# Optimization experiments

Hardware: AMD Instinct MI355X
Metric: run time of the kernel (lower is better)

Reference implementation:

```python
import jax, jax.numpy as jnp
import numpy as np

B, S, ENC = 16, 1500, 1280      # batch, audio frames, encoder dim
K = 2                            # pool stride -> in_dim = ENC*K
IN_DIM = ENC * K                 # 2560
LLM = 2048                       # output dim
HID = 512                        # expert hidden dim
E, TOPK = 8, 2                   # num experts, top-k
EPS = 1e-6


def _ln(x, g, b):
    m = jnp.mean(x, -1, keepdims=True)
    v = jnp.mean((x - m) ** 2, -1, keepdims=True)
    return (x - m) * jax.lax.rsqrt(v + EPS) * g + b


def _swiglu(x, w12, w3):
    # w12: [2H, D], w3: [O, H]; dropout is identity at inference
    h = x @ w12.T
    gate, val = jnp.split(h, 2, axis=-1)
    return (jax.nn.silu(gate) * val) @ w3.T


def setup_inputs() -> dict:
    key = jax.random.key(0)
    ks = jax.random.split(key, 12)
    sc = 0.02
    return {
        "x": jax.random.normal(ks[0], (B, S, ENC), jnp.float32),
        "ln_pre_g": 1.0 + sc * jax.random.normal(ks[1], (IN_DIM,), jnp.float32),
        "ln_pre_b": sc * jax.random.normal(ks[2], (IN_DIM,), jnp.float32),
        "router_w": sc * jax.random.normal(ks[3], (E, IN_DIM), jnp.float32),
        "router_b": sc * jax.random.normal(ks[4], (E,), jnp.float32),
        "shared_w12": sc * jax.random.normal(ks[5], (2 * HID, IN_DIM), jnp.float32),
        "shared_w3": sc * jax.random.normal(ks[6], (LLM, HID), jnp.float32),
        "experts_w12": sc * jax.random.normal(ks[7], (E, 2 * HID, IN_DIM), jnp.float32),
        "experts_w3": sc * jax.random.normal(ks[8], (E, LLM, HID), jnp.float32),
        "ln_post_g": 1.0 + sc * jax.random.normal(ks[9], (LLM,), jnp.float32),
        "ln_post_b": sc * jax.random.normal(ks[10], (LLM,), jnp.float32),
    }


def reference(x, ln_pre_g, ln_pre_b, router_w, router_b,
              shared_w12, shared_w3, experts_w12, experts_w3,
              ln_post_g, ln_post_b):
    b, s, d = x.shape
    pad = (-s) % K
    if pad:
        x = jnp.pad(x, ((0, 0), (0, pad), (0, 0)))
    xk = x.reshape(b, -1, d * K)          # [B, S/K, IN_DIM]
    new_s = xk.shape[1]
    nx = _ln(xk.reshape(-1, d * K), ln_pre_g, ln_pre_b)   # [T, IN_DIM]

    shared = _swiglu(nx, shared_w12, shared_w3)            # [T, LLM]

    logits = nx @ router_w.T + router_b                    # [T, E]
    probs = jax.nn.softmax(logits, -1)
    w, idx = jax.lax.top_k(probs, TOPK)                    # [T, K]
    w = w / (jnp.sum(w, -1, keepdims=True) + 1e-20)
    # combine[t, e] = sum_k w[t,k] * (idx[t,k]==e)  (equiv to masked loop + scatter-add)
    combine = jnp.sum(jax.nn.one_hot(idx, E, dtype=nx.dtype) * w[..., None], axis=1)  # [T, E]

    hid = jnp.einsum('td,efd->tef', nx, experts_w12)       # [T, E, 2H]
    gate, val = jnp.split(hid, 2, axis=-1)
    act = jax.nn.silu(gate) * val                          # [T, E, H]
    eo = jnp.einsum('teh,eoh->teo', act, experts_w3)       # [T, E, LLM]
    routed = jnp.einsum('teo,te->to', eo, combine)         # [T, LLM]

    out = _ln(shared + routed, ln_post_g, ln_post_b)
    return out.reshape(b, new_s, LLM)
```

## Files before the change

kernel.cpp:

```cpp
#include <hip/hip_runtime.h>

#define T_TOK 12000
#define NSLOT 24000
#define DIN 2560
#define DH 512
#define DOUT 2048
#define NEXP 8
#define MSH 12000
#define SHBASE 24000

typedef unsigned short u16;
typedef unsigned int u32;
typedef __attribute__((ext_vector_type(4))) float f32x4;
typedef __attribute__((ext_vector_type(8))) short short8;
typedef __attribute__((ext_vector_type(4))) u16 u16x4;
typedef __attribute__((ext_vector_type(8))) u16 u16x8;

__device__ __forceinline__ u16 f2bf(float f) {
  u32 u = __builtin_bit_cast(u32, f);
  return (u16)((u + 0x7fffu + ((u >> 16) & 1u)) >> 16);
}
__device__ __forceinline__ float bf2f(u16 h) {
  return __builtin_bit_cast(float, (u32)h << 16);
}

__device__ __forceinline__ void gload_lds16(const void* g, void* l) {
  __builtin_amdgcn_global_load_lds((const __attribute__((address_space(1))) u32*)g,
                                   (__attribute__((address_space(3))) u32*)l, 16, 0, 0);
}

__global__ __launch_bounds__(256) void cvt_bf16_kernel(const float* __restrict__ in,
                                                       u16* __restrict__ out, int n4) {
  const int i = blockIdx.x * 256 + threadIdx.x;
  if (i >= n4) return;
  f32x4 v = ((const f32x4*)in)[i];
  u16x4 o = { f2bf(v.x), f2bf(v.y), f2bf(v.z), f2bf(v.w) };
  ((u16x4*)out)[i] = o;
}

__global__ __launch_bounds__(256) void ln_router_kernel(
    const float* __restrict__ x, const float* __restrict__ gamma, const float* __restrict__ beta,
    const float* __restrict__ rw, const float* __restrict__ rb,
    u16* __restrict__ nx, int* __restrict__ tok_e, float* __restrict__ tok_w,
    int* __restrict__ count) {
  const int t = blockIdx.x * 4 + (threadIdx.x >> 6);
  const int lane = threadIdx.x & 63;
  const f32x4* xrow = (const f32x4*)(x + (size_t)t * DIN);

  f32x4 xv[10];
  float s = 0.f, s2 = 0.f;
#pragma unroll
  for (int c = 0; c < 10; ++c) {
    xv[c] = xrow[c * 64 + lane];
#pragma unroll
    for (int i = 0; i < 4; ++i) { s += xv[c][i]; s2 += xv[c][i] * xv[c][i]; }
  }
#pragma unroll
  for (int off = 32; off > 0; off >>= 1) {
    s += __shfl_xor(s, off);
    s2 += __shfl_xor(s2, off);
  }
  const float mean = s * (1.0f / DIN);
  const float var = s2 * (1.0f / DIN) - mean * mean;
  const float rstd = rsqrtf(var + 1e-6f);

  u16* nxrow = nx + (size_t)t * DIN;
#pragma unroll
  for (int c = 0; c < 10; ++c) {
    f32x4 g = ((const f32x4*)gamma)[c * 64 + lane];
    f32x4 b = ((const f32x4*)beta)[c * 64 + lane];
    xv[c] = (xv[c] - mean) * rstd * g + b;
    u16x4 p = { f2bf(xv[c].x), f2bf(xv[c].y), f2bf(xv[c].z), f2bf(xv[c].w) };
    ((u16x4*)nxrow)[c * 64 + lane] = p;
  }

  float lp[NEXP];
#pragma unroll
  for (int e = 0; e < NEXP; ++e) {
    const f32x4* rwe = (const f32x4*)(rw + (size_t)e * DIN);
    float acc = 0.f;
#pragma unroll
    for (int c = 0; c < 10; ++c) {
      f32x4 r = rwe[c * 64 + lane];
      acc += xv[c].x * r.x + xv[c].y * r.y + xv[c].z * r.z + xv[c].w * r.w;
    }
    lp[e] = acc;
  }
#pragma unroll
  for (int e = 0; e < NEXP; ++e)
#pragma unroll
    for (int off = 32; off > 0; off >>= 1) lp[e] += __shfl_xor(lp[e], off);

  if (lane == 0) {
    float lg[NEXP];
#pragma unroll
    for (int e = 0; e < NEXP; ++e) lg[e] = lp[e] + rb[e];
    float mx = lg[0];
#pragma unroll
    for (int e = 1; e < NEXP; ++e) mx = fmaxf(mx, lg[e]);
    float p[NEXP], ps = 0.f;
#pragma unroll
    for (int e = 0; e < NEXP; ++e) { p[e] = expf(lg[e] - mx); ps += p[e]; }
    int i0 = 0;
#pragma unroll
    for (int e = 1; e < NEXP; ++e) if (p[e] > p[i0]) i0 = e;
    int i1 = (i0 == 0) ? 1 : 0;
#pragma unroll
    for (int e = 0; e < NEXP; ++e) if (e != i0 && p[e] > p[i1]) i1 = e;
    float w0 = p[i0] / ps, w1 = p[i1] / ps;
    const float inv = 1.0f / (w0 + w1 + 1e-20f);
    w0 *= inv; w1 *= inv;
    tok_e[2 * t] = i0; tok_e[2 * t + 1] = i1;
    tok_w[2 * t] = w0; tok_w[2 * t + 1] = w1;
    atomicAdd(&count[i0 * 32], 1);
    atomicAdd(&count[i1 * 32], 1);
  }
}

__global__ void prefix_kernel(const int* __restrict__ count, int* __restrict__ prefix) {
  if (threadIdx.x == 0) {
    int acc = 0;
    for (int e = 0; e < NEXP; ++e) { prefix[e] = acc; acc += count[e * 32]; }
  }
}

__global__ __launch_bounds__(256) void assign_kernel(
    const int* __restrict__ tok_e, const float* __restrict__ tok_w, const int* __restrict__ prefix,
    int* __restrict__ cursor, int* __restrict__ slot_token, float* __restrict__ slot_w,
    int* __restrict__ token_slot) {
  const int t = blockIdx.x * 256 + threadIdx.x;
  if (t >= T_TOK) return;
#pragma unroll
  for (int k = 0; k < 2; ++k) {
    const int e = tok_e[2 * t + k];
    const int pos = atomicAdd(&cursor[e * 32], 1);
    const int sl = prefix[e] + pos;
    slot_token[sl] = t;
    slot_w[sl] = tok_w[2 * t + k];
    token_slot[2 * t + k] = sl;
  }
}

__global__ __launch_bounds__(256, 2) void gemm_ffn1(
    const u16* __restrict__ A0, const u16* __restrict__ Bsh, const u16* __restrict__ Bex,
    u16* __restrict__ ACT,
    const int* __restrict__ cnt32, const int* __restrict__ prefix,
    const int* __restrict__ slot_token) {
  constexpr int K = 2560;
  constexpr int NX = 8;
  __shared__ u16 ldsA[128 * 64];
  __shared__ u16 ldsG[64 * 64];
  __shared__ u16 ldsV[64 * 64];

  int A_act = 0;
#pragma unroll
  for (int ee = 0; ee < 9; ++ee) {
    const int c = (ee == 8) ? MSH : cnt32[ee * 32];
    A_act += ((c + 127) >> 7) * NX;
  }
  const int bid = blockIdx.x;
  if (bid >= A_act) return;

  const int xcd = bid & 7, rank = bid >> 3;
  const int q = A_act >> 3, r = A_act & 7;
  const int tile = (xcd < r ? xcd * (q + 1) : r * (q + 1) + (xcd - r) * q) + rank;

  int e = 8, local = 0, m_valid = MSH, row_off = 0;
  {
    int bacc = 0, found = 0;
#pragma unroll
    for (int ee = 0; ee < 9; ++ee) {
      const int c = (ee == 8) ? MSH : cnt32[ee * 32];
      const int w = ((c + 127) >> 7) * NX;
      if (!found && tile < bacc + w) {
        found = 1; e = ee; local = tile - bacc; m_valid = c;
        row_off = (ee == 8) ? 0 : prefix[ee];
      }
      bacc += w;
    }
  }
  const int ty = local / NX;
  const int tx = local % NX;
  const int crow_base = (e == 8) ? SHBASE : row_off;
  const u16* Bb = (e == 8) ? Bsh : Bex + (size_t)e * 1024 * K;

  const int tid = threadIdx.x;
  const int lane = tid & 63;
  const int wid = tid >> 6;
  const int sk8 = ((lane & 7) ^ (lane >> 3)) * 8;

  const u16* aptr[4];
#pragma unroll
  for (int i = 0; i < 4; ++i) {
    const int rr = wid * 32 + i * 8 + (lane >> 3);
    int gr = ty * 128 + rr;
    gr = gr < m_valid ? gr : (m_valid - 1);
    const int ar = (e == 8) ? gr : slot_token[row_off + gr];
    aptr[i] = A0 + (size_t)ar * K;
  }
  const u16* gptr[2];
  const u16* vptr[2];
#pragma unroll
  for (int j = 0; j < 2; ++j) {
    const int rr = wid * 16 + j * 8 + (lane >> 3);
    gptr[j] = Bb + (size_t)(tx * 64 + rr) * K;
    vptr[j] = Bb + (size_t)(512 + tx * 64 + rr) * K;
  }

  const f32x4 zero = {0.f, 0.f, 0.f, 0.f};
  f32x4 accg[4][2], accv[4][2];
#pragma unroll
  for (int m = 0; m < 4; ++m)
#pragma unroll
    for (int n = 0; n < 2; ++n) { accg[m][n] = zero; accv[m][n] = zero; }

  const int wr = (wid >> 1) * 64;
  const int wc = (wid & 1) * 32;
  const int fr = lane & 15;
  const int fk = (lane >> 4) * 8;

  for (int k0 = 0; k0 < K; k0 += 64) {
#pragma unroll
    for (int i = 0; i < 4; ++i)
      gload_lds16(aptr[i] + k0 + sk8, &ldsA[(wid * 4 + i) * 512]);
#pragma unroll
    for (int j = 0; j < 2; ++j) {
      gload_lds16(gptr[j] + k0 + sk8, &ldsG[(wid * 2 + j) * 512]);
      gload_lds16(vptr[j] + k0 + sk8, &ldsV[(wid * 2 + j) * 512]);
    }
    __syncthreads();
#pragma unroll
    for (int kk = 0; kk < 2; ++kk) {
      short8 af[4], bg[2], bv[2];
      const int kbs = (kk * 32 + fk) ^ ((lane & 7) << 3);
#pragma unroll
      for (int m = 0; m < 4; ++m)
        af[m] = *(const short8*)&ldsA[(wr + m * 16 + fr) * 64 + kbs];
#pragma unroll
      for (int n = 0; n < 2; ++n) {
        bg[n] = *(const short8*)&ldsG[(wc + n * 16 + fr) * 64 + kbs];
        bv[n] = *(const short8*)&ldsV[(wc + n * 16 + fr) * 64 + kbs];
      }
#pragma unroll
      for (int m = 0; m < 4; ++m)
#pragma unroll
        for (int n = 0; n < 2; ++n) {
          accg[m][n] = __builtin_amdgcn_mfma_f32_16x16x32_bf16(af[m], bg[n], accg[m][n], 0, 0, 0);
          accv[m][n] = __builtin_amdgcn_mfma_f32_16x16x32_bf16(af[m], bv[n], accv[m][n], 0, 0, 0);
        }
    }
    __syncthreads();
  }

  const int ccol = tx * 64 + wc + (lane & 15);
#pragma unroll
  for (int m = 0; m < 4; ++m) {
#pragma unroll
    for (int i = 0; i < 4; ++i) {
      const int row = wr + m * 16 + (lane >> 4) * 4 + i;
      const int gr = ty * 128 + row;
      if (gr < m_valid) {
        u16* crow = ACT + (size_t)(crow_base + gr) * DH;
#pragma unroll
        for (int n = 0; n < 2; ++n) {
          const float g = accg[m][n][i];
          const float v = accv[m][n][i];
          const float sig = 1.0f / (1.0f + __expf(-g));
          crow[ccol + n * 16] = f2bf(g * sig * v);
        }
      }
    }
  }
}

__global__ __launch_bounds__(256, 2) void gemm_ffn2(
    const u16* __restrict__ A0, const u16* __restrict__ Bsh, const u16* __restrict__ Bex,
    u16* __restrict__ C,
    const int* __restrict__ cnt32, const int* __restrict__ prefix,
    const float* __restrict__ slot_w) {
  constexpr int N = 2048;
  constexpr int K = 512;
  constexpr int NX = 16;
  __shared__ u16 ldsA[128 * 64];
  __shared__ u16 ldsB[128 * 64];

  int A_act = 0;
#pragma unroll
  for (int ee = 0; ee < 9; ++ee) {
    const int c = (ee == 8) ? MSH : cnt32[ee * 32];
    A_act += ((c + 127) >> 7) * NX;
  }
  const int bid = blockIdx.x;
  if (bid >= A_act) return;

  const int xcd = bid & 7, rank = bid >> 3;
  const int q = A_act >> 3, r = A_act & 7;
  const int tile = (xcd < r ? xcd * (q + 1) : r * (q + 1) + (xcd - r) * q) + rank;

  int e = 8, local = 0, m_valid = MSH, row_off = 0;
  {
    int bacc = 0, found = 0;
#pragma unroll
    for (int ee = 0; ee < 9; ++ee) {
      const int c = (ee == 8) ? MSH : cnt32[ee * 32];
      const int w = ((c + 127) >> 7) * NX;
      if (!found && tile < bacc + w) {
        found = 1; e = ee; local = tile - bacc; m_valid = c;
        row_off = (ee == 8) ? 0 : prefix[ee];
      }
      bacc += w;
    }
  }
  const int ty = local / NX;
  const int tx = local % NX;
  const int crow_base = (e == 8) ? SHBASE : row_off;
  const u16* Bb = (e == 8) ? Bsh : Bex + (size_t)e * N * K;

  const int tid = threadIdx.x;
  const int lane = tid & 63;
  const int wid = tid >> 6;
  const int sk8 = ((lane & 7) ^ (lane >> 3)) * 8;

  const u16* aptr[4];
  const u16* bptr[4];
#pragma unroll
  for (int i = 0; i < 4; ++i) {
    const int rr = wid * 32 + i * 8 + (lane >> 3);
    int gr = ty * 128 + rr;
    gr = gr < m_valid ? gr : (m_valid - 1);
    aptr[i] = A0 + (size_t)(crow_base + gr) * K;
    bptr[i] = Bb + (size_t)(tx * 128 + rr) * K;
  }

  const f32x4 zero = {0.f, 0.f, 0.f, 0.f};
  f32x4 acc[4][4];
#pragma unroll
  for (int m = 0; m < 4; ++m)
#pragma unroll
    for (int n = 0; n < 4; ++n) acc[m][n] = zero;

  const int wr = (wid >> 1) * 64;
  const int wc = (wid & 1) * 64;
  const int fr = lane & 15;
  const int fk = (lane >> 4) * 8;

  for (int k0 = 0; k0 < K; k0 += 64) {
#pragma unroll
    for (int i = 0; i < 4; ++i) {
      gload_lds16(aptr[i] + k0 + sk8, &ldsA[(wid * 4 + i) * 512]);
      gload_lds16(bptr[i] + k0 + sk8, &ldsB[(wid * 4 + i) * 512]);
    }
    __syncthreads();
#pragma unroll
    for (int kk = 0; kk < 2; ++kk) {
      short8 af[4], bfm[4];
      const int kbs = (kk * 32 + fk) ^ ((lane & 7) << 3);
#pragma unroll
      for (int m = 0; m < 4; ++m)
        af[m] = *(const short8*)&ldsA[(wr + m * 16 + fr) * 64 + kbs];
#pragma unroll
      for (int n = 0; n < 4; ++n)
        bfm[n] = *(const short8*)&ldsB[(wc + n * 16 + fr) * 64 + kbs];
#pragma unroll
      for (int m = 0; m < 4; ++m)
#pragma unroll
        for (int n = 0; n < 4; ++n)
          acc[m][n] = __builtin_amdgcn_mfma_f32_16x16x32_bf16(af[m], bfm[n], acc[m][n], 0, 0, 0);
    }
    __syncthreads();
  }

  const int ccol = wc + (lane & 15);
#pragma unroll
  for (int m = 0; m < 4; ++m) {
#pragma unroll
    for (int i = 0; i < 4; ++i) {
      const int row = wr + m * 16 + (lane >> 4) * 4 + i;
      const int gr = ty * 128 + row;
      if (gr < m_valid) {
        const float wscale = (e == 8) ? 1.0f : slot_w[row_off + gr];
        u16* crow = C + (size_t)(crow_base + gr) * N + tx * 128;
#pragma unroll
        for (int n = 0; n < 4; ++n) crow[ccol + n * 16] = f2bf(acc[m][n][i] * wscale);
      }
    }
  }
}

__global__ __launch_bounds__(256) void final_ln_kernel(
    const u16* __restrict__ O16, const int* __restrict__ token_slot,
    const float* __restrict__ gamma, const float* __restrict__ beta, float* __restrict__ out) {
  const int t = blockIdx.x;
  const int tid = threadIdx.x;
  const int lane = tid & 63;
  const int wv = tid >> 6;
  const int s0 = token_slot[2 * t], s1 = token_slot[2 * t + 1];
  const int c = tid * 8;
  u16x8 a8 = *(const u16x8*)&O16[(size_t)(SHBASE + t) * DOUT + c];
  u16x8 b8 = *(const u16x8*)&O16[(size_t)s0 * DOUT + c];
  u16x8 c8 = *(const u16x8*)&O16[(size_t)s1 * DOUT + c];
  float v[8];
  float s = 0.f, s2 = 0.f;
#pragma unroll
  for (int i = 0; i < 8; ++i) {
    v[i] = bf2f(a8[i]) + bf2f(b8[i]) + bf2f(c8[i]);
    s += v[i];
    s2 += v[i] * v[i];
  }
#pragma unroll
  for (int off = 32; off > 0; off >>= 1) {
    s += __shfl_xor(s, off);
    s2 += __shfl_xor(s2, off);
  }
  __shared__ float red[4][2];
  if (lane == 0) { red[wv][0] = s; red[wv][1] = s2; }
  __syncthreads();
  const float S = red[0][0] + red[1][0] + red[2][0] + red[3][0];
  const float S2 = red[0][1] + red[1][1] + red[2][1] + red[3][1];
  const float mean = S * (1.0f / DOUT);
  const float var = S2 * (1.0f / DOUT) - mean * mean;
  const float rstd = rsqrtf(var + 1e-6f);
  f32x4 g0 = ((const f32x4*)gamma)[tid * 2], g1 = ((const f32x4*)gamma)[tid * 2 + 1];
  f32x4 be0 = ((const f32x4*)beta)[tid * 2], be1 = ((const f32x4*)beta)[tid * 2 + 1];
  f32x4 o0, o1;
#pragma unroll
  for (int i = 0; i < 4; ++i) {
    o0[i] = (v[i] - mean) * rstd * g0[i] + be0[i];
    o1[i] = (v[4 + i] - mean) * rstd * g1[i] + be1[i];
  }
  f32x4* orow = (f32x4*)(out + (size_t)t * DOUT);
  orow[tid * 2] = o0;
  orow[tid * 2 + 1] = o1;
}

extern "C" void kernel_launch(void* const* d_in, const int* in_sizes, int n_in,
                              void* d_out, int out_size, void* d_ws, size_t ws_size,
                              hipStream_t stream) {
  (void)in_sizes; (void)n_in; (void)out_size; (void)ws_size;
  const float* x = (const float*)d_in[0];
  const float* ln_pre_g = (const float*)d_in[1];
  const float* ln_pre_b = (const float*)d_in[2];
  const float* router_w = (const float*)d_in[3];
  const float* router_b = (const float*)d_in[4];
  const float* shared_w12 = (const float*)d_in[5];
  const float* shared_w3 = (const float*)d_in[6];
  const float* experts_w12 = (const float*)d_in[7];
  const float* experts_w3 = (const float*)d_in[8];
  const float* ln_post_g = (const float*)d_in[9];
  const float* ln_post_b = (const float*)d_in[10];
  float* out = (float*)d_out;

  size_t off = 0;
  char* ws = (char*)d_ws;
  auto take = [&](size_t bytes) -> void* {
    void* p = ws + off;
    off += (bytes + 255) & ~(size_t)255;
    return p;
  };
  u16* w12s = (u16*)take((size_t)1024 * 2560 * 2);
  u16* w3s  = (u16*)take((size_t)2048 * 512 * 2);
  u16* ew12 = (u16*)take((size_t)NEXP * 1024 * 2560 * 2);
  u16* ew3  = (u16*)take((size_t)NEXP * 2048 * 512 * 2);
  u16* nx   = (u16*)take((size_t)T_TOK * DIN * 2);
  u16* act  = (u16*)take((size_t)36000 * DH * 2);
  u16* O16  = (u16*)take((size_t)36000 * DOUT * 2);
  int* tok_e = (int*)take(NSLOT * 4);
  float* tok_w = (float*)take(NSLOT * 4);
  int* slot_token = (int*)take(NSLOT * 4);
  float* slot_w = (float*)take(NSLOT * 4);
  int* token_slot = (int*)take(NSLOT * 4);
  int* cnt = (int*)take(3 * 8 * 32 * 4);
  int* cursor = cnt + 8 * 32;
  int* prefix = cnt + 2 * 8 * 32;

  hipMemsetAsync(cnt, 0, 3 * 8 * 32 * 4, stream);

  cvt_bf16_kernel<<<(1024 * 2560 / 4 + 255) / 256, 256, 0, stream>>>(shared_w12, w12s, 1024 * 2560 / 4);
  cvt_bf16_kernel<<<(2048 * 512 / 4 + 255) / 256, 256, 0, stream>>>(shared_w3, w3s, 2048 * 512 / 4);
  cvt_bf16_kernel<<<(NEXP * 1024 * 2560 / 4 + 255) / 256, 256, 0, stream>>>(experts_w12, ew12, NEXP * 1024 * 2560 / 4);
  cvt_bf16_kernel<<<(NEXP * 2048 * 512 / 4 + 255) / 256, 256, 0, stream>>>(experts_w3, ew3, NEXP * 2048 * 512 / 4);

  ln_router_kernel<<<T_TOK / 4, 256, 0, stream>>>(x, ln_pre_g, ln_pre_b, router_w, router_b,
                                                  nx, tok_e, tok_w, cnt);
  prefix_kernel<<<1, 64, 0, stream>>>(cnt, prefix);
  assign_kernel<<<(T_TOK + 255) / 256, 256, 0, stream>>>(tok_e, tok_w, prefix, cursor,
                                                         slot_token, slot_w, token_slot);

  gemm_ffn1<<<289 * 8, 256, 0, stream>>>(nx, w12s, ew12, act, cnt, prefix, slot_token);
  gemm_ffn2<<<289 * 16, 256, 0, stream>>>(act, w3s, ew3, O16, cnt, prefix, slot_w);

  final_ln_kernel<<<T_TOK, 256, 0, stream>>>(O16, token_slot, ln_post_g, ln_post_b, out);
}
```

Baseline: 584.6 us.

## Fuse weight conversions, stage router weights in LDS, retile FFN1, warp-per-token final LN

The four weight-conversion launches become one kernel that picks its source and destination by index range, cutting launch overhead. The router dot product now stages router weights through shared memory once per block instead of each wave reading them from global, at the cost of extra barriers. FFN1 tiles are reordered into groups of four N-tiles per M-stripe so A rows are reused in cache. Final LayerNorm maps one wave to each token, dropping the block-wide shared-memory reduction and barrier.

```diff
diff --git a/kernel.cpp b/kernel.cpp
--- a/kernel.cpp
+++ b/kernel.cpp
@@ -29,13 +29,24 @@
                                    (__attribute__((address_space(3))) u32*)l, 16, 0, 0);
 }
 
-__global__ __launch_bounds__(256) void cvt_bf16_kernel(const float* __restrict__ in,
-                                                       u16* __restrict__ out, int n4) {
-  const int i = blockIdx.x * 256 + threadIdx.x;
-  if (i >= n4) return;
-  f32x4 v = ((const f32x4*)in)[i];
+#define CN0 655360
+#define CN1 262144
+#define CN2 5242880
+#define CN3 2097152
+__global__ __launch_bounds__(256) void cvt4_kernel(
+    const float* __restrict__ s0, u16* __restrict__ d0,
+    const float* __restrict__ s1, u16* __restrict__ d1,
+    const float* __restrict__ s2, u16* __restrict__ d2,
+    const float* __restrict__ s3, u16* __restrict__ d3) {
+  int i = blockIdx.x * 256 + threadIdx.x;
+  const float* s; u16* d;
+  if (i < CN0) { s = s0; d = d0; }
+  else if (i < CN0 + CN1) { i -= CN0; s = s1; d = d1; }
+  else if (i < CN0 + CN1 + CN2) { i -= CN0 + CN1; s = s2; d = d2; }
+  else { i -= CN0 + CN1 + CN2; if (i >= CN3) return; s = s3; d = d3; }
+  f32x4 v = ((const f32x4*)s)[i];
   u16x4 o = { f2bf(v.x), f2bf(v.y), f2bf(v.z), f2bf(v.w) };
-  ((u16x4*)out)[i] = o;
+  ((u16x4*)d)[i] = o;
 }
 
 __global__ __launch_bounds__(256) void ln_router_kernel(
@@ -43,9 +54,12 @@
     const float* __restrict__ rw, const float* __restrict__ rb,
     u16* __restrict__ nx, int* __restrict__ tok_e, float* __restrict__ tok_w,
     int* __restrict__ count) {
-  const int t = blockIdx.x * 4 + (threadIdx.x >> 6);
-  const int lane = threadIdx.x & 63;
+  const int tid = threadIdx.x;
+  const int t = blockIdx.x * 4 + (tid >> 6);
+  const int lane = tid & 63;
   const f32x4* xrow = (const f32x4*)(x + (size_t)t * DIN);
+
+  __shared__ float rwl[NEXP][256];
 
   f32x4 xv[10];
   float s = 0.f, s2 = 0.f;
@@ -76,15 +90,18 @@
 
   float lp[NEXP];
 #pragma unroll
-  for (int e = 0; e < NEXP; ++e) {
-    const f32x4* rwe = (const f32x4*)(rw + (size_t)e * DIN);
-    float acc = 0.f;
-#pragma unroll
-    for (int c = 0; c < 10; ++c) {
-      f32x4 r = rwe[c * 64 + lane];
-      acc += xv[c].x * r.x + xv[c].y * r.y + xv[c].z * r.z + xv[c].w * r.w;
-    }
-    lp[e] = acc;
+  for (int e = 0; e < NEXP; ++e) lp[e] = 0.f;
+#pragma unroll
+  for (int c = 0; c < 10; ++c) {
+    __syncthreads();
+#pragma unroll
+    for (int e = 0; e < NEXP; ++e) rwl[e][tid] = rw[(size_t)e * DIN + c * 256 + tid];
+    __syncthreads();
+#pragma unroll
+    for (int e = 0; e < NEXP; ++e) {
+      f32x4 r = *(const f32x4*)&rwl[e][lane * 4];
+      lp[e] += xv[c].x * r.x + xv[c].y * r.y + xv[c].z * r.z + xv[c].w * r.w;
+    }
   }
 #pragma unroll
   for (int e = 0; e < NEXP; ++e)
@@ -165,22 +182,26 @@
   const int q = A_act >> 3, r = A_act & 7;
   const int tile = (xcd < r ? xcd * (q + 1) : r * (q + 1) + (xcd - r) * q) + rank;
 
-  int e = 8, local = 0, m_valid = MSH, row_off = 0;
+  int e = 8, local = 0, m_valid = MSH, row_off = 0, nty = (MSH + 127) >> 7;
   {
     int bacc = 0, found = 0;
 #pragma unroll
     for (int ee = 0; ee < 9; ++ee) {
       const int c = (ee == 8) ? MSH : cnt32[ee * 32];
-      const int w = ((c + 127) >> 7) * NX;
+      const int nt = (c + 127) >> 7;
+      const int w = nt * NX;
       if (!found && tile < bacc + w) {
-        found = 1; e = ee; local = tile - bacc; m_valid = c;
+        found = 1; e = ee; local = tile - bacc; m_valid = c; nty = nt;
         row_off = (ee == 8) ? 0 : prefix[ee];
       }
       bacc += w;
     }
   }
-  const int ty = local / NX;
-  const int tx = local % NX;
+  const int nty4 = nty * 4;
+  const int xs = local / nty4;
+  const int rem = local - xs * nty4;
+  const int ty = rem >> 2;
+  const int tx = (xs << 2) + (rem & 3);
   const int crow_base = (e == 8) ? SHBASE : row_off;
   const u16* Bb = (e == 8) ? Bsh : Bex + (size_t)e * 1024 * K;
 
@@ -390,47 +411,53 @@
 __global__ __launch_bounds__(256) void final_ln_kernel(
     const u16* __restrict__ O16, const int* __restrict__ token_slot,
     const float* __restrict__ gamma, const float* __restrict__ beta, float* __restrict__ out) {
-  const int t = blockIdx.x;
-  const int tid = threadIdx.x;
-  const int lane = tid & 63;
-  const int wv = tid >> 6;
+  const int t = blockIdx.x * 4 + (threadIdx.x >> 6);
+  const int lane = threadIdx.x & 63;
   const int s0 = token_slot[2 * t], s1 = token_slot[2 * t + 1];
-  const int c = tid * 8;
-  u16x8 a8 = *(const u16x8*)&O16[(size_t)(SHBASE + t) * DOUT + c];
-  u16x8 b8 = *(const u16x8*)&O16[(size_t)s0 * DOUT + c];
-  u16x8 c8 = *(const u16x8*)&O16[(size_t)s1 * DOUT + c];
-  float v[8];
+  const u16* rsh = O16 + (size_t)(SHBASE + t) * DOUT;
+  const u16* r0 = O16 + (size_t)s0 * DOUT;
+  const u16* r1 = O16 + (size_t)s1 * DOUT;
+
+  float v[32];
   float s = 0.f, s2 = 0.f;
 #pragma unroll
-  for (int i = 0; i < 8; ++i) {
-    v[i] = bf2f(a8[i]) + bf2f(b8[i]) + bf2f(c8[i]);
-    s += v[i];
-    s2 += v[i] * v[i];
+  for (int c = 0; c < 4; ++c) {
+    const int col = c * 512 + lane * 8;
+    u16x8 a8 = *(const u16x8*)&rsh[col];
+    u16x8 b8 = *(const u16x8*)&r0[col];
+    u16x8 c8 = *(const u16x8*)&r1[col];
+#pragma unroll
+    for (int i = 0; i < 8; ++i) {
+      const float x = bf2f(a8[i]) + bf2f(b8[i]) + bf2f(c8[i]);
+      v[c * 8 + i] = x;
+      s += x;
+      s2 += x * x;
+    }
   }
 #pragma unroll
   for (int off = 32; off > 0; off >>= 1) {
     s += __shfl_xor(s, off);
     s2 += __shfl_xor(s2, off);
   }
-  __shared__ float red[4][2];
-  if (lane == 0) { red[wv][0] = s; red[wv][1] = s2; }
-  __syncthreads();
-  const float S = red[0][0] + red[1][0] + red[2][0] + red[3][0];
-  const float S2 = red[0][1] + red[1][1] + red[2][1] + red[3][1];
-  const float mean = S * (1.0f / DOUT);
-  const float var = S2 * (1.0f / DOUT) - mean * mean;
+  const float mean = s * (1.0f / DOUT);
+  const float var = s2 * (1.0f / DOUT) - mean * mean;
   const float rstd = rsqrtf(var + 1e-6f);
-  f32x4 g0 = ((const f32x4*)gamma)[tid * 2], g1 = ((const f32x4*)gamma)[tid * 2 + 1];
-  f32x4 be0 = ((const f32x4*)beta)[tid * 2], be1 = ((const f32x4*)beta)[tid * 2 + 1];
-  f32x4 o0, o1;
-#pragma unroll
-  for (int i = 0; i < 4; ++i) {
-    o0[i] = (v[i] - mean) * rstd * g0[i] + be0[i];
-    o1[i] = (v[4 + i] - mean) * rstd * g1[i] + be1[i];
-  }
-  f32x4* orow = (f32x4*)(out + (size_t)t * DOUT);
-  orow[tid * 2] = o0;
-  orow[tid * 2 + 1] = o1;
+
+  float* orow = out + (size_t)t * DOUT;
+#pragma unroll
+  for (int c = 0; c < 4; ++c) {
+    const int col = c * 512 + lane * 8;
+    f32x4 g0 = ((const f32x4*)gamma)[col >> 2], g1 = ((const f32x4*)gamma)[(col >> 2) + 1];
+    f32x4 b0 = ((const f32x4*)beta)[col >> 2],  b1 = ((const f32x4*)beta)[(col >> 2) + 1];
+    f32x4 o0, o1;
+#pragma unroll
+    for (int i = 0; i < 4; ++i) {
+      o0[i] = (v[c * 8 + i] - mean) * rstd * g0[i] + b0[i];
+      o1[i] = (v[c * 8 + 4 + i] - mean) * rstd * g1[i] + b1[i];
+    }
+    *(f32x4*)&orow[col] = o0;
+    *(f32x4*)&orow[col + 4] = o1;
+  }
 }
 
 extern "C" void kernel_launch(void* const* d_in, const int* in_sizes, int n_in,
@@ -475,10 +502,8 @@
 
   hipMemsetAsync(cnt, 0, 3 * 8 * 32 * 4, stream);
 
-  cvt_bf16_kernel<<<(1024 * 2560 / 4 + 255) / 256, 256, 0, stream>>>(shared_w12, w12s, 1024 * 2560 / 4);
-  cvt_bf16_kernel<<<(2048 * 512 / 4 + 255) / 256, 256, 0, stream>>>(shared_w3, w3s, 2048 * 512 / 4);
-  cvt_bf16_kernel<<<(NEXP * 1024 * 2560 / 4 + 255) / 256, 256, 0, stream>>>(experts_w12, ew12, NEXP * 1024 * 2560 / 4);
-  cvt_bf16_kernel<<<(NEXP * 2048 * 512 / 4 + 255) / 256, 256, 0, stream>>>(experts_w3, ew3, NEXP * 2048 * 512 / 4);
+  cvt4_kernel<<<(CN0 + CN1 + CN2 + CN3) / 256, 256, 0, stream>>>(
+      shared_w12, w12s, shared_w3, w3s, experts_w12, ew12, experts_w3, ew3);
 
   ln_router_kernel<<<T_TOK / 4, 256, 0, stream>>>(x, ln_pre_g, ln_pre_b, router_w, router_b,
                                                   nx, tok_e, tok_w, cnt);
@@ -489,5 +514,5 @@
   gemm_ffn1<<<289 * 8, 256, 0, stream>>>(nx, w12s, ew12, act, cnt, prefix, slot_token);
   gemm_ffn2<<<289 * 16, 256, 0, stream>>>(act, w3s, ew3, O16, cnt, prefix, slot_w);
 
-  final_ln_kernel<<<T_TOK, 256, 0, stream>>>(O16, token_slot, ln_post_g, ln_post_b, out);
-}
+  final_ln_kernel<<<T_TOK / 4, 256, 0, stream>>>(O16, token_slot, ln_post_g, ln_post_b, out);
+}
```

New measurement: 547.9 us. -6.3%, faster.
